# Kernel optimization log

Hardware: AMD Instinct MI355X
Metric: run time of the kernel (lower is better)

## Reference

```python
import jax, jax.numpy as jnp
import numpy as np

N = 8192
D = 512
EPS = 1e-12  # F.normalize default eps


def setup_inputs() -> dict:
    key = jax.random.key(0)
    k1, k2 = jax.random.split(key)
    cur = jax.random.normal(k1, (N, D), dtype=jnp.float32)
    # randn -> mixed-sign entries, so every row of (incidence_m > 0) is unique
    # (the only case where the original `incidence_m += head` shapes agree).
    incidence_m = jax.random.normal(k2, (N, N), dtype=jnp.float32)
    return {"cur": cur, "incidence_m": incidence_m}


def reference(cur, incidence_m):
    # construct_directed: dedup rows of (incidence_m > 0); with all rows unique,
    # each node is its own hyperedge leader and head == mask as float, row order
    # preserved. head is built from python ints in torch, hence non-differentiable.
    mask = incidence_m > 0
    head = jax.lax.stop_gradient(mask.astype(incidence_m.dtype))  # [N, N]
    # F.normalize(head, dim=-1): L2 per row with eps clamp
    head = head / jnp.maximum(
        jnp.sqrt(jnp.sum(head * head, axis=-1, keepdims=True)), EPS
    )
    inc = incidence_m + head                          # [N, N]
    edge_fea = inc @ cur                              # [N, D]
    edge_degree = jnp.sum(inc, axis=-1, keepdims=True)  # [N, 1]
    return edge_fea / edge_degree
```

## Files before the change

### kernel.cpp

```cpp
#include <hip/hip_runtime.h>
#include <stdint.h>


#define NROWS 8192
#define DDIM  512

typedef float f32x4 __attribute__((ext_vector_type(4)));
typedef short s16x8 __attribute__((ext_vector_type(8)));

__device__ __forceinline__ unsigned short f2bf(float f) {
  union { float f; unsigned int u; } c; c.f = f;
  unsigned int u = c.u;
  unsigned int r = u + 0x7FFFu + ((u >> 16) & 1u);
  return (unsigned short)(r >> 16);
}

__global__ __launch_bounds__(256) void bprep_kernel(const float* __restrict__ cur,
                                                    unsigned char* __restrict__ bws) {
  int idx = blockIdx.x * 256 + threadIdx.x;
  int n = idx & 511;
  int kg9 = idx >> 9;
  int kt = kg9 >> 3;
  int kg = kg9 & 7;
  int k0 = kt * 64 + kg * 8;
  union { unsigned short h[8]; uint4 q; } u;
#pragma unroll
  for (int e = 0; e < 8; ++e)
    u.h[e] = f2bf(cur[(size_t)(k0 + e) * DDIM + n]);
  int nt = n >> 8, nn = n & 255;
  size_t off = ((size_t)(nt * 128 + kt) << 15) + ((size_t)kg << 12) + ((size_t)nn << 4);
  *(uint4*)(bws + off) = u.q;
}


#define FENCE() __builtin_amdgcn_sched_barrier(0)
#define BARRIER() __builtin_amdgcn_s_barrier()
#define WAITLGKM() asm volatile("s_waitcnt lgkmcnt(0)" ::: "memory")

__global__ __launch_bounds__(256, 2) void gemm_kernel(const float* __restrict__ inc,
                                                      const unsigned char* __restrict__ bws,
                                                      float* __restrict__ out) {
  __shared__ __align__(16) unsigned char smem[16640];
  unsigned char* const aBuf0 = smem;
  unsigned char* const aBuf1 = smem + 4096;
  unsigned char* const mBuf0 = smem + 8192;
  unsigned char* const mBuf1 = smem + 12288;

  const int tid = threadIdx.x;
  const int lane = tid & 63;
  const int wv = tid >> 6;
  const int id = blockIdx.x;
  const int nt = (id >> 2) & 1;
  const int mt = (id >> 3) * 4 + (id & 3);
  const int brow = mt * 32;
  const int bcol = nt * 256;

  const int sm = tid >> 3;
  const int sp = tid & 7;
  const float4* gAr = (const float4*)(inc + (size_t)(brow + sm) * NROWS) + sp * 2;
  const int aWr = (sp << 9) + ((sm ^ sp) << 4);

  const unsigned char* gBb = bws + ((size_t)(nt * 128) << 15);

  int aOff[2][2];
  int bOff[8];
#pragma unroll
  for (int kh = 0; kh < 2; ++kh) {
    int kg = kh * 4 + (lane >> 4);
#pragma unroll
    for (int g = 0; g < 2; ++g) {
      int r = g * 16 + (lane & 15);
      aOff[kh][g] = (kg << 9) + ((r ^ kg) << 4);
    }
#pragma unroll
    for (int cg = 0; cg < 4; ++cg)
      bOff[kh * 4 + cg] = (kg << 12) + ((wv * 64 + cg * 16 + (lane & 15)) << 4);
  }

  f32x4 acc1[2][4], acc2[2][4];
#pragma unroll
  for (int a = 0; a < 2; ++a)
#pragma unroll
    for (int b = 0; b < 4; ++b) {
      acc1[a][b] = (f32x4){0.f, 0.f, 0.f, 0.f};
      acc2[a][b] = (f32x4){0.f, 0.f, 0.f, 0.f};
    }

  double s1d = 0.0;
  int cnt = 0;
  float4 x0, x1, y0, y1;
  s16x8 bA[8], bB[8];

#define ISSUE_A(d0, d1, KT) do { d0 = gAr[(KT) * 16]; d1 = gAr[(KT) * 16 + 1]; } while (0)

#define LOADB(BS, KT) do {                                                                \
    const unsigned char* _g = gBb + ((size_t)(KT) << 15);                                 \
    _Pragma("unroll")                                                                     \
    for (int _i = 0; _i < 8; ++_i) BS[_i] = *(const s16x8*)(_g + bOff[_i]);               \
  } while (0)

#define XFORM(s0, s1, ADST, MDST) do {                                                    \
    s1d += (double)s0.x + (double)s0.y + (double)s0.z + (double)s0.w;                     \
    s1d += (double)s1.x + (double)s1.y + (double)s1.z + (double)s1.w;                     \
    cnt += (s0.x > 0.f) + (s0.y > 0.f) + (s0.z > 0.f) + (s0.w > 0.f);                     \
    cnt += (s1.x > 0.f) + (s1.y > 0.f) + (s1.z > 0.f) + (s1.w > 0.f);                     \
    uint4 _a, _m;                                                                         \
    asm("v_cvt_pk_bf16_f32 %0, %1, %2" : "=v"(_a.x) : "v"(s0.x), "v"(s0.y));              \
    asm("v_cvt_pk_bf16_f32 %0, %1, %2" : "=v"(_a.y) : "v"(s0.z), "v"(s0.w));              \
    asm("v_cvt_pk_bf16_f32 %0, %1, %2" : "=v"(_a.z) : "v"(s1.x), "v"(s1.y));              \
    asm("v_cvt_pk_bf16_f32 %0, %1, %2" : "=v"(_a.w) : "v"(s1.z), "v"(s1.w));              \
    _m.x = (s0.x > 0.f ? 0x3F80u : 0u) | (s0.y > 0.f ? 0x3F800000u : 0u);                 \
    _m.y = (s0.z > 0.f ? 0x3F80u : 0u) | (s0.w > 0.f ? 0x3F800000u : 0u);                 \
    _m.z = (s1.x > 0.f ? 0x3F80u : 0u) | (s1.y > 0.f ? 0x3F800000u : 0u);                 \
    _m.w = (s1.z > 0.f ? 0x3F80u : 0u) | (s1.w > 0.f ? 0x3F800000u : 0u);                 \
    *(uint4*)((ADST) + aWr) = _a;                                                         \
    *(uint4*)((MDST) + aWr) = _m;                                                         \
  } while (0)

#define MFMA_TILE(AC, MC, BS) do {                                                        \
    __builtin_amdgcn_s_setprio(1);                                                        \
    _Pragma("unroll")                                                                     \
    for (int kh = 0; kh < 2; ++kh) {                                                      \
      s16x8 af[2], am[2];                                                                 \
      _Pragma("unroll")                                                                   \
      for (int g = 0; g < 2; ++g) af[g] = *(const s16x8*)((AC) + aOff[kh][g]);            \
      _Pragma("unroll")                                                                   \
      for (int g = 0; g < 2; ++g) am[g] = *(const s16x8*)((MC) + aOff[kh][g]);            \
      _Pragma("unroll")                                                                   \
      for (int rg = 0; rg < 2; ++rg)                                                      \
        _Pragma("unroll")                                                                 \
        for (int cg = 0; cg < 4; ++cg) {                                                  \
          acc1[rg][cg] = __builtin_amdgcn_mfma_f32_16x16x32_bf16(af[rg], BS[kh * 4 + cg], \
                                                                 acc1[rg][cg], 0, 0, 0); \
          acc2[rg][cg] = __builtin_amdgcn_mfma_f32_16x16x32_bf16(am[rg], BS[kh * 4 + cg], \
                                                                 acc2[rg][cg], 0, 0, 0); \
        }                                                                                 \
    }                                                                                     \
    __builtin_amdgcn_s_setprio(0);                                                        \
  } while (0)

#define SYNC() do { FENCE(); WAITLGKM(); FENCE(); BARRIER(); FENCE(); } while (0)

  ISSUE_A(x0, x1, 0);
  LOADB(bA, 0);
  ISSUE_A(y0, y1, 1);
  XFORM(x0, x1, aBuf0, mBuf0);
  SYNC();

  for (int kt = 0; kt < 126; kt += 2) {
    ISSUE_A(x0, x1, kt + 2);
    LOADB(bB, kt + 1);
    FENCE();
    MFMA_TILE(aBuf0, mBuf0, bA);
    XFORM(y0, y1, aBuf1, mBuf1);
    SYNC();
    ISSUE_A(y0, y1, kt + 3);
    LOADB(bA, kt + 2);
    FENCE();
    MFMA_TILE(aBuf1, mBuf1, bB);
    XFORM(x0, x1, aBuf0, mBuf0);
    SYNC();
  }

  LOADB(bB, 127);
  FENCE();
  MFMA_TILE(aBuf0, mBuf0, bA);
  XFORM(y0, y1, aBuf1, mBuf1);
  SYNC();
  MFMA_TILE(aBuf1, mBuf1, bB);

#pragma unroll
  for (int o = 1; o < 8; o <<= 1) {
    s1d += __shfl_xor(s1d, o);
    cnt += __shfl_xor(cnt, o);
  }
  __syncthreads();
  float* const invsS = (float*)aBuf0;
  float* const rdegS = invsS + 32;
  if (sp == 0) {
    double sq = sqrt((double)cnt);
    invsS[sm] = (cnt > 0) ? (float)(1.0 / sq) : 0.0f;
    rdegS[sm] = (float)(1.0 / (s1d + sq));
  }
  __syncthreads();

#pragma unroll
  for (int rg = 0; rg < 2; ++rg) {
    int rb = rg * 16 + ((lane >> 4) << 2);
#pragma unroll
    for (int cg = 0; cg < 4; ++cg) {
      int col = bcol + wv * 64 + cg * 16 + (lane & 15);
#pragma unroll
      for (int r = 0; r < 4; ++r) {
        int rl = rb + r;
        out[(size_t)(brow + rl) * DDIM + col] =
            (acc1[rg][cg][r] + invsS[rl] * acc2[rg][cg][r]) * rdegS[rl];
      }
    }
  }
#undef ISSUE_A
#undef LOADB
#undef XFORM
#undef MFMA_TILE
#undef SYNC
}

extern "C" void kernel_launch(void* const* d_in, const int* in_sizes, int n_in,
                              void* d_out, int out_size, void* d_ws, size_t ws_size,
                              hipStream_t stream) {
  const float* cur = (const float*)d_in[0];
  const float* incm = (const float*)d_in[1];
  float* out = (float*)d_out;
  unsigned char* bws = (unsigned char*)d_ws;

  hipLaunchKernelGGL(bprep_kernel, dim3((NROWS * DDIM / 8) / 256), dim3(256), 0, stream,
                     cur, bws);
  hipLaunchKernelGGL(gemm_kernel, dim3(512), dim3(256), 0, stream, incm, bws, out);
}
```

Baseline: 184.3 us.

## Halve GEMM row tile to 16 and double grid for higher occupancy

Shrinks each block's M tile from 32 to 16 rows, which halves LDS use, accumulators and per-thread A loads. The grid doubles to 1024 blocks and launch bounds now allow 4 blocks per SIMD group. Block-to-tile mapping is remapped with a new swizzled LDS layout and 8-byte stores. The aim is more waves in flight to hide the memory latency of streaming the fp32 incidence matrix, at the cost of loading the B tiles twice as often per output and doing less MFMA work per B load.

```diff
diff --git a/kernel.cpp b/kernel.cpp
--- a/kernel.cpp
+++ b/kernel.cpp
@@ -37,61 +37,57 @@
 #define BARRIER() __builtin_amdgcn_s_barrier()
 #define WAITLGKM() asm volatile("s_waitcnt lgkmcnt(0)" ::: "memory")
 
-__global__ __launch_bounds__(256, 2) void gemm_kernel(const float* __restrict__ inc,
+__global__ __launch_bounds__(256, 4) void gemm_kernel(const float* __restrict__ inc,
                                                       const unsigned char* __restrict__ bws,
                                                       float* __restrict__ out) {
-  __shared__ __align__(16) unsigned char smem[16640];
+  __shared__ __align__(16) unsigned char smem[8192];
   unsigned char* const aBuf0 = smem;
-  unsigned char* const aBuf1 = smem + 4096;
-  unsigned char* const mBuf0 = smem + 8192;
-  unsigned char* const mBuf1 = smem + 12288;
+  unsigned char* const aBuf1 = smem + 2048;
+  unsigned char* const mBuf0 = smem + 4096;
+  unsigned char* const mBuf1 = smem + 6144;
 
   const int tid = threadIdx.x;
   const int lane = tid & 63;
   const int wv = tid >> 6;
   const int id = blockIdx.x;
-  const int nt = (id >> 2) & 1;
-  const int mt = (id >> 3) * 4 + (id & 3);
-  const int brow = mt * 32;
+  const int nt = id & 1;
+  const int mt = ((id >> 1) & 3) * 128 + ((id >> 3) & 31) * 4 + (id >> 8);
+  const int brow = mt * 16;
   const int bcol = nt * 256;
 
-  const int sm = tid >> 3;
-  const int sp = tid & 7;
-  const float4* gAr = (const float4*)(inc + (size_t)(brow + sm) * NROWS) + sp * 2;
-  const int aWr = (sp << 9) + ((sm ^ sp) << 4);
+  const int sm = tid >> 4;
+  const int sp = tid & 15;
+  const int kgw = sp >> 1, half = sp & 1;
+  const float4* gAr = (const float4*)(inc + (size_t)(brow + sm) * NROWS) + sp;
+  const int aWr = (kgw << 8) + (((sm ^ kgw) & 15) << 4) + (half << 3);
 
   const unsigned char* gBb = bws + ((size_t)(nt * 128) << 15);
 
-  int aOff[2][2];
+  int aOff[2];
   int bOff[8];
 #pragma unroll
   for (int kh = 0; kh < 2; ++kh) {
     int kg = kh * 4 + (lane >> 4);
-#pragma unroll
-    for (int g = 0; g < 2; ++g) {
-      int r = g * 16 + (lane & 15);
-      aOff[kh][g] = (kg << 9) + ((r ^ kg) << 4);
-    }
+    int r = lane & 15;
+    aOff[kh] = (kg << 8) + (((r ^ kg) & 15) << 4);
 #pragma unroll
     for (int cg = 0; cg < 4; ++cg)
       bOff[kh * 4 + cg] = (kg << 12) + ((wv * 64 + cg * 16 + (lane & 15)) << 4);
   }
 
-  f32x4 acc1[2][4], acc2[2][4];
-#pragma unroll
-  for (int a = 0; a < 2; ++a)
-#pragma unroll
-    for (int b = 0; b < 4; ++b) {
-      acc1[a][b] = (f32x4){0.f, 0.f, 0.f, 0.f};
-      acc2[a][b] = (f32x4){0.f, 0.f, 0.f, 0.f};
-    }
+  f32x4 acc1[4], acc2[4];
+#pragma unroll
+  for (int b = 0; b < 4; ++b) {
+    acc1[b] = (f32x4){0.f, 0.f, 0.f, 0.f};
+    acc2[b] = (f32x4){0.f, 0.f, 0.f, 0.f};
+  }
 
   double s1d = 0.0;
   int cnt = 0;
-  float4 x0, x1, y0, y1;
+  float4 x, y;
   s16x8 bA[8], bB[8];
 
-#define ISSUE_A(d0, d1, KT) do { d0 = gAr[(KT) * 16]; d1 = gAr[(KT) * 16 + 1]; } while (0)
+#define ISSUE_A(d, KT) do { d = gAr[(KT) * 16]; } while (0)
 
 #define LOADB(BS, KT) do {                                                                \
     const unsigned char* _g = gBb + ((size_t)(KT) << 15);                                 \
@@ -99,84 +95,75 @@
     for (int _i = 0; _i < 8; ++_i) BS[_i] = *(const s16x8*)(_g + bOff[_i]);               \
   } while (0)
 
-#define XFORM(s0, s1, ADST, MDST) do {                                                    \
+#define XFORM(s0, ADST, MDST) do {                                                        \
     s1d += (double)s0.x + (double)s0.y + (double)s0.z + (double)s0.w;                     \
-    s1d += (double)s1.x + (double)s1.y + (double)s1.z + (double)s1.w;                     \
     cnt += (s0.x > 0.f) + (s0.y > 0.f) + (s0.z > 0.f) + (s0.w > 0.f);                     \
-    cnt += (s1.x > 0.f) + (s1.y > 0.f) + (s1.z > 0.f) + (s1.w > 0.f);                     \
-    uint4 _a, _m;                                                                         \
-    asm("v_cvt_pk_bf16_f32 %0, %1, %2" : "=v"(_a.x) : "v"(s0.x), "v"(s0.y));              \
-    asm("v_cvt_pk_bf16_f32 %0, %1, %2" : "=v"(_a.y) : "v"(s0.z), "v"(s0.w));              \
-    asm("v_cvt_pk_bf16_f32 %0, %1, %2" : "=v"(_a.z) : "v"(s1.x), "v"(s1.y));              \
-    asm("v_cvt_pk_bf16_f32 %0, %1, %2" : "=v"(_a.w) : "v"(s1.z), "v"(s1.w));              \
-    _m.x = (s0.x > 0.f ? 0x3F80u : 0u) | (s0.y > 0.f ? 0x3F800000u : 0u);                 \
-    _m.y = (s0.z > 0.f ? 0x3F80u : 0u) | (s0.w > 0.f ? 0x3F800000u : 0u);                 \
-    _m.z = (s1.x > 0.f ? 0x3F80u : 0u) | (s1.y > 0.f ? 0x3F800000u : 0u);                 \
-    _m.w = (s1.z > 0.f ? 0x3F80u : 0u) | (s1.w > 0.f ? 0x3F800000u : 0u);                 \
-    *(uint4*)((ADST) + aWr) = _a;                                                         \
-    *(uint4*)((MDST) + aWr) = _m;                                                         \
+    unsigned dlo, dhi;                                                                    \
+    asm("v_cvt_pk_bf16_f32 %0, %1, %2" : "=v"(dlo) : "v"(s0.x), "v"(s0.y));               \
+    asm("v_cvt_pk_bf16_f32 %0, %1, %2" : "=v"(dhi) : "v"(s0.z), "v"(s0.w));               \
+    unsigned mlo = (s0.x > 0.f ? 0x3F80u : 0u) | (s0.y > 0.f ? 0x3F800000u : 0u);         \
+    unsigned mhi = (s0.z > 0.f ? 0x3F80u : 0u) | (s0.w > 0.f ? 0x3F800000u : 0u);         \
+    *(unsigned long long*)((ADST) + aWr) =                                                \
+        (unsigned long long)dlo | ((unsigned long long)dhi << 32);                        \
+    *(unsigned long long*)((MDST) + aWr) =                                                \
+        (unsigned long long)mlo | ((unsigned long long)mhi << 32);                        \
   } while (0)
 
 #define MFMA_TILE(AC, MC, BS) do {                                                        \
     __builtin_amdgcn_s_setprio(1);                                                        \
     _Pragma("unroll")                                                                     \
     for (int kh = 0; kh < 2; ++kh) {                                                      \
-      s16x8 af[2], am[2];                                                                 \
+      s16x8 af = *(const s16x8*)((AC) + aOff[kh]);                                        \
+      s16x8 am = *(const s16x8*)((MC) + aOff[kh]);                                        \
       _Pragma("unroll")                                                                   \
-      for (int g = 0; g < 2; ++g) af[g] = *(const s16x8*)((AC) + aOff[kh][g]);            \
-      _Pragma("unroll")                                                                   \
-      for (int g = 0; g < 2; ++g) am[g] = *(const s16x8*)((MC) + aOff[kh][g]);            \
-      _Pragma("unroll")                                                                   \
-      for (int rg = 0; rg < 2; ++rg)                                                      \
-        _Pragma("unroll")                                                                 \
-        for (int cg = 0; cg < 4; ++cg) {                                                  \
-          acc1[rg][cg] = __builtin_amdgcn_mfma_f32_16x16x32_bf16(af[rg], BS[kh * 4 + cg], \
-                                                                 acc1[rg][cg], 0, 0, 0); \
-          acc2[rg][cg] = __builtin_amdgcn_mfma_f32_16x16x32_bf16(am[rg], BS[kh * 4 + cg], \
-                                                                 acc2[rg][cg], 0, 0, 0); \
-        }                                                                                 \
+      for (int cg = 0; cg < 4; ++cg) {                                                    \
+        acc1[cg] = __builtin_amdgcn_mfma_f32_16x16x32_bf16(af, BS[kh * 4 + cg],           \
+                                                           acc1[cg], 0, 0, 0);           \
+        acc2[cg] = __builtin_amdgcn_mfma_f32_16x16x32_bf16(am, BS[kh * 4 + cg],           \
+                                                           acc2[cg], 0, 0, 0);           \
+      }                                                                                   \
     }                                                                                     \
     __builtin_amdgcn_s_setprio(0);                                                        \
   } while (0)
 
 #define SYNC() do { FENCE(); WAITLGKM(); FENCE(); BARRIER(); FENCE(); } while (0)
 
-  ISSUE_A(x0, x1, 0);
+  ISSUE_A(x, 0);
   LOADB(bA, 0);
-  ISSUE_A(y0, y1, 1);
-  XFORM(x0, x1, aBuf0, mBuf0);
+  ISSUE_A(y, 1);
+  XFORM(x, aBuf0, mBuf0);
   SYNC();
 
   for (int kt = 0; kt < 126; kt += 2) {
-    ISSUE_A(x0, x1, kt + 2);
+    ISSUE_A(x, kt + 2);
     LOADB(bB, kt + 1);
     FENCE();
     MFMA_TILE(aBuf0, mBuf0, bA);
-    XFORM(y0, y1, aBuf1, mBuf1);
+    XFORM(y, aBuf1, mBuf1);
     SYNC();
-    ISSUE_A(y0, y1, kt + 3);
+    ISSUE_A(y, kt + 3);
     LOADB(bA, kt + 2);
     FENCE();
     MFMA_TILE(aBuf1, mBuf1, bB);
-    XFORM(x0, x1, aBuf0, mBuf0);
+    XFORM(x, aBuf0, mBuf0);
     SYNC();
   }
 
   LOADB(bB, 127);
   FENCE();
   MFMA_TILE(aBuf0, mBuf0, bA);
-  XFORM(y0, y1, aBuf1, mBuf1);
+  XFORM(y, aBuf1, mBuf1);
   SYNC();
   MFMA_TILE(aBuf1, mBuf1, bB);
 
 #pragma unroll
-  for (int o = 1; o < 8; o <<= 1) {
+  for (int o = 1; o < 16; o <<= 1) {
     s1d += __shfl_xor(s1d, o);
     cnt += __shfl_xor(cnt, o);
   }
   __syncthreads();
   float* const invsS = (float*)aBuf0;
-  float* const rdegS = invsS + 32;
+  float* const rdegS = invsS + 16;
   if (sp == 0) {
     double sq = sqrt((double)cnt);
     invsS[sm] = (cnt > 0) ? (float)(1.0 / sq) : 0.0f;
@@ -184,9 +171,8 @@
   }
   __syncthreads();
 
-#pragma unroll
-  for (int rg = 0; rg < 2; ++rg) {
-    int rb = rg * 16 + ((lane >> 4) << 2);
+  {
+    int rb = (lane >> 4) << 2;
 #pragma unroll
     for (int cg = 0; cg < 4; ++cg) {
       int col = bcol + wv * 64 + cg * 16 + (lane & 15);
@@ -194,7 +180,7 @@
       for (int r = 0; r < 4; ++r) {
         int rl = rb + r;
         out[(size_t)(brow + rl) * DDIM + col] =
-            (acc1[rg][cg][r] + invsS[rl] * acc2[rg][cg][r]) * rdegS[rl];
+            (acc1[cg][r] + invsS[rl] * acc2[cg][r]) * rdegS[rl];
       }
     }
   }
@@ -215,5 +201,5 @@
 
   hipLaunchKernelGGL(bprep_kernel, dim3((NROWS * DDIM / 8) / 256), dim3(256), 0, stream,
                      cur, bws);
-  hipLaunchKernelGGL(gemm_kernel, dim3(512), dim3(256), 0, stream, incm, bws, out);
-}
+  hipLaunchKernelGGL(gemm_kernel, dim3(1024), dim3(256), 0, stream, incm, bws, out);
+}
```

Result: slower. 441.5 us (+139.5%).
